# Optimization experiments

Hardware: AMD Instinct MI355X
Metric: run time of the kernel (lower is better)

Reference implementation:

```python
import jax, jax.numpy as jnp
import numpy as np

# static config (matches init_kwargs and a standard 4-level FPN for ~800px input)
SPATIAL_SHAPES = ((100, 100), (50, 50), (25, 25), (13, 13))  # (H_l, W_l)
B, C, H, L, P = 2, 256, 8, 4, 4
DFFN = 2048
DH = C // H
LQ = sum(h * w for h, w in SPATIAL_SHAPES)  # 13294


def layer_norm(x, g, b, eps=1e-5):
    m = jnp.mean(x, -1, keepdims=True)
    v = jnp.mean((x - m) ** 2, -1, keepdims=True)
    return (x - m) * jax.lax.rsqrt(v + eps) * g + b


def ms_deform_sample(value, loc, attn):
    # value [B,Lv,H,DH], loc [B,Lq,H,L,P,2] in [0,1], attn [B,Lq,H,L,P]
    value = jnp.transpose(value, (0, 2, 1, 3))  # [B,H,Lv,DH]
    lq = loc.shape[1]
    out = jnp.zeros((B, H, lq, DH), value.dtype)
    start = 0
    for l, (Hl, Wl) in enumerate(SPATIAL_SHAPES):
        v = jax.lax.dynamic_slice_in_dim(value, start, Hl * Wl, axis=2)  # [B,H,N_l,DH]
        # grid_sample(align_corners=False) coords: x = loc_x*W - 0.5
        gx = jnp.transpose(loc[:, :, :, l, :, 0], (0, 2, 1, 3)) * Wl - 0.5  # [B,H,Lq,P]
        gy = jnp.transpose(loc[:, :, :, l, :, 1], (0, 2, 1, 3)) * Hl - 0.5
        aw = jnp.transpose(attn[:, :, :, l, :], (0, 2, 1, 3))  # [B,H,Lq,P]
        x0 = jnp.floor(gx)
        y0 = jnp.floor(gy)
        for dx in (0.0, 1.0):
            for dy in (0.0, 1.0):
                xi = x0 + dx
                yi = y0 + dy
                w = (1.0 - jnp.abs(gx - xi)) * (1.0 - jnp.abs(gy - yi))
                valid = (xi >= 0) & (xi < Wl) & (yi >= 0) & (yi < Hl)
                idx = (jnp.clip(yi, 0, Hl - 1) * Wl + jnp.clip(xi, 0, Wl - 1)).astype(jnp.int32)
                g = jnp.take_along_axis(v, idx.reshape(B, H, -1)[..., None], axis=2)  # [B,H,Lq*P,DH]
                ww = (w * aw * valid.astype(w.dtype))[..., None]  # [B,H,Lq,P,1]
                out = out + jnp.sum(g.reshape(B, H, lq, P, DH) * ww, axis=3)
        start += Hl * Wl
    return jnp.transpose(out, (0, 2, 1, 3)).reshape(B, lq, C)


def setup_inputs() -> dict:
    key = jax.random.key(0)
    ks = jax.random.split(key, 16)
    s = 0.02
    return {
        "src": jax.random.normal(ks[0], (B, LQ, C), jnp.float32),
        "pos": jax.random.normal(ks[1], (B, LQ, C), jnp.float32),
        "reference_points": jax.random.uniform(ks[2], (B, LQ, L, 2), jnp.float32),
        "w_value": jax.random.normal(ks[3], (C, C), jnp.float32) * s,
        "b_value": jnp.zeros((C,), jnp.float32),
        "w_off": jax.random.normal(ks[4], (C, H * L * P * 2), jnp.float32) * s,
        "b_off": jax.random.normal(ks[5], (H * L * P * 2,), jnp.float32) * s,
        "w_attn": jax.random.normal(ks[6], (C, H * L * P), jnp.float32) * s,
        "b_attn": jnp.zeros((H * L * P,), jnp.float32),
        "w_out": jax.random.normal(ks[7], (C, C), jnp.float32) * s,
        "b_out": jnp.zeros((C,), jnp.float32),
        "ln1_g": jnp.ones((C,), jnp.float32),
        "ln1_b": jnp.zeros((C,), jnp.float32),
        "w_ffn1": jax.random.normal(ks[8], (C, DFFN), jnp.float32) * s,
        "b_ffn1": jnp.zeros((DFFN,), jnp.float32),
        "w_ffn2": jax.random.normal(ks[9], (DFFN, C), jnp.float32) * s,
        "b_ffn2": jnp.zeros((C,), jnp.float32),
        "ln2_g": jnp.ones((C,), jnp.float32),
        "ln2_b": jnp.zeros((C,), jnp.float32),
    }


def reference(src, pos, reference_points, w_value, b_value, w_off, b_off, w_attn, b_attn,
              w_out, b_out, ln1_g, ln1_b, w_ffn1, b_ffn1, w_ffn2, b_ffn2, ln2_g, ln2_b):
    # DeformableTransformerEncoderLayer.forward (eval mode, no dropout)
    q = src + pos  # with_pos_embed
    lq = q.shape[1]
    value = (src @ w_value + b_value).reshape(B, -1, H, DH)
    off = (q @ w_off + b_off).reshape(B, lq, H, L, P, 2)
    attn = (q @ w_attn + b_attn).reshape(B, lq, H, L * P)
    attn = jax.nn.softmax(attn, axis=-1).reshape(B, lq, H, L, P)
    # offset_normalizer = (W_l, H_l)
    norm = jnp.array([[w, h] for h, w in SPATIAL_SHAPES], dtype=src.dtype)
    loc = reference_points[:, :, None, :, None, :] + off / norm[None, None, None, :, None, :]
    src2 = ms_deform_sample(value, loc, attn) @ w_out + b_out
    x = layer_norm(src + src2, ln1_g, ln1_b)
    ff = jax.nn.relu(x @ w_ffn1 + b_ffn1) @ w_ffn2 + b_ffn2
    return layer_norm(x + ff, ln2_g, ln2_b)
```

## Files before the change

kernel.cpp:

```cpp
#include <hip/hip_runtime.h>

#define LQN   13294
#define NBAT  2
#define MROWS (NBAT * LQN)
#define CCH   256
#define NHEAD 8
#define DHEAD 32
#define NLVL  4
#define NPT   4
#define DFF   2048

typedef short short8 __attribute__((ext_vector_type(8)));
typedef float f32x4 __attribute__((ext_vector_type(4)));
typedef unsigned short u16;
typedef u16 u16x4 __attribute__((ext_vector_type(4)));

__device__ __forceinline__ u16 f2bf(float f) {
  unsigned int u = __builtin_bit_cast(unsigned int, f);
  u += 0x7fffu + ((u >> 16) & 1u);
  return (u16)(u >> 16);
}
__device__ __forceinline__ float bf2f(u16 s) {
  unsigned int u = ((unsigned int)s) << 16;
  return __builtin_bit_cast(float, u);
}
__device__ __forceinline__ void async16(const void* g, void* l) {
  __builtin_amdgcn_global_load_lds(
      (const __attribute__((address_space(1))) void*)g,
      (__attribute__((address_space(3))) void*)l, 16, 0, 0);
}

template<int OUT_MODE>
__global__ __launch_bounds__(256, 2)
void gemm_bf16(const u16* __restrict__ A, const u16* __restrict__ BT,
               const float* __restrict__ bias, void* __restrict__ Cout,
               int M, int N, int K)
{
  __shared__ u16 As[2][128 * 64];
  __shared__ u16 Bs[2][128 * 64];
  const int t    = threadIdx.x;
  const int lane = t & 63;
  const int wid  = t >> 6;
  const int wm   = wid >> 1, wn = wid & 1;
  const int bm   = blockIdx.x, bn = blockIdx.y;
  const int l15  = lane & 15;
  const int kq   = lane >> 4;

  f32x4 acc[4][4];
#pragma unroll
  for (int m = 0; m < 4; ++m)
#pragma unroll
    for (int n = 0; n < 4; ++n) acc[m][n] = (f32x4)0.0f;

  auto stage = [&](int buf, int kt) {
#pragma unroll
    for (int i = 0; i < 4; ++i) {
      const int c   = i * 256 + t;
      const int row = c >> 3;
      const int kg  = (c & 7) ^ (row & 7);
      int ar = bm * 128 + row; ar = ar < M ? ar : M - 1;
      async16(&A[(size_t)ar * K + kt + kg * 8], &As[buf][c * 8]);
      const int br = bn * 128 + row;
      async16(&BT[(size_t)br * K + kt + kg * 8], &Bs[buf][c * 8]);
    }
  };

  stage(0, 0);
  __syncthreads();
  int cur = 0;

  for (int kt = 0; kt < K; kt += 64) {
    if (kt + 64 < K) stage(cur ^ 1, kt + 64);

#pragma unroll
    for (int kk = 0; kk < 2; ++kk) {
      short8 af[4], bfr[4];
#pragma unroll
      for (int m = 0; m < 4; ++m) {
        const int row = wm * 64 + m * 16 + l15;
        const int xb  = (kk * 64 + kq * 16) ^ ((row & 7) << 4);
        af[m] = *(const short8*)((const char*)&As[cur][0] + row * 128 + xb);
      }
#pragma unroll
      for (int n = 0; n < 4; ++n) {
        const int col = wn * 64 + n * 16 + l15;
        const int xb  = (kk * 64 + kq * 16) ^ ((col & 7) << 4);
        bfr[n] = *(const short8*)((const char*)&Bs[cur][0] + col * 128 + xb);
      }
#pragma unroll
      for (int m = 0; m < 4; ++m)
#pragma unroll
        for (int n = 0; n < 4; ++n)
          acc[m][n] = __builtin_amdgcn_mfma_f32_16x16x32_bf16(af[m], bfr[n], acc[m][n], 0, 0, 0);
    }

    __syncthreads();
    cur ^= 1;
  }

  const int crow0 = bm * 128 + wm * 64;
  const int ccol0 = bn * 128 + wn * 64;
#pragma unroll
  for (int n = 0; n < 4; ++n) {
    int col = ccol0 + n * 16 + l15;
    float bv = bias[col];
#pragma unroll
    for (int m = 0; m < 4; ++m) {
      int rbase = crow0 + m * 16 + kq * 4;
#pragma unroll
      for (int j = 0; j < 4; ++j) {
        int row = rbase + j;
        if (row < M) {
          float v = acc[m][n][j] + bv;
          if constexpr (OUT_MODE == 0) {
            ((float*)Cout)[(size_t)row * N + col] = v;
          } else {
            if constexpr (OUT_MODE == 2) v = fmaxf(v, 0.0f);
            ((u16*)Cout)[(size_t)row * N + col] = f2bf(v);
          }
        }
      }
    }
  }
}

__global__ __launch_bounds__(512, 2)
void ffn_fused(const u16* __restrict__ x_bf, const u16* __restrict__ W1T,
               const u16* __restrict__ W2T, const float* __restrict__ b1,
               const float* __restrict__ b2, float* __restrict__ out)
{
  extern __shared__ char smem[];
  u16* w1s = (u16*)(smem);
  u16* w2s = (u16*)(smem + 65536);
  char* ps = (char*)(smem + 131072);

  const int t    = threadIdx.x;
  const int lane = t & 63;
  const int wid  = t >> 6;
  const int l15  = lane & 15;
  const int kq   = lane >> 4;
  const int bm   = blockIdx.x;
  const int pwm  = wid >> 1, pwn = wid & 1;
  const int wm   = wid >> 2, wn = wid & 3;

  short8 xr[2][8];
#pragma unroll
  for (int m = 0; m < 2; ++m) {
    int ar = bm * 128 + pwm * 32 + m * 16 + l15;
    ar = ar < MROWS ? ar : MROWS - 1;
    const char* xb = (const char*)x_bf + (size_t)ar * 512 + kq * 16;
#pragma unroll
    for (int ks = 0; ks < 8; ++ks)
      xr[m][ks] = *(const short8*)(xb + ks * 64);
  }

  auto stage = [&](int buf, int it) {
#pragma unroll
    for (int i = 0; i < 4; ++i) {
      const int c  = i * 512 + t;
      const int r1 = c >> 5;
      const int k1 = ((c & 31) ^ (r1 & 7)) * 8;
      async16(&W1T[(size_t)(it * 64 + r1) * 256 + k1], &w1s[buf * 16384 + c * 8]);
      const int r2 = c >> 3;
      const int k2 = ((c & 7) ^ (r2 & 7)) * 8;
      async16(&W2T[(size_t)r2 * 2048 + it * 64 + k2], &w2s[buf * 16384 + c * 8]);
    }
  };

  f32x4 acc[4][4];
#pragma unroll
  for (int m = 0; m < 4; ++m)
#pragma unroll
    for (int n = 0; n < 4; ++n) acc[m][n] = (f32x4)0.0f;

  stage(0, 0);
  __syncthreads();

  for (int it = 0; it < 32; ++it) {
    const int cur = it & 1;
    if (it < 31) stage(cur ^ 1, it + 1);

    f32x4 p[2][2];
#pragma unroll
    for (int m = 0; m < 2; ++m)
#pragma unroll
      for (int n = 0; n < 2; ++n) p[m][n] = (f32x4)0.0f;

#pragma unroll
    for (int ks = 0; ks < 8; ++ks) {
      short8 bfr[2];
#pragma unroll
      for (int n = 0; n < 2; ++n) {
        const int wrow = pwn * 32 + n * 16 + l15;
        const int xb   = (ks * 64 + kq * 16) ^ ((wrow & 7) << 4);
        bfr[n] = *(const short8*)((const char*)&w1s[cur * 16384] + wrow * 512 + xb);
      }
#pragma unroll
      for (int m = 0; m < 2; ++m)
#pragma unroll
        for (int n = 0; n < 2; ++n)
          p[m][n] = __builtin_amdgcn_mfma_f32_16x16x32_bf16(xr[m][ks], bfr[n], p[m][n], 0, 0, 0);
    }

#pragma unroll
    for (int n = 0; n < 2; ++n) {
      const int col = pwn * 32 + n * 16 + l15;
      const float bv = b1[it * 64 + col];
      const int chnk = col >> 3;
      const int sub  = (col & 7) * 2;
#pragma unroll
      for (int m = 0; m < 2; ++m)
#pragma unroll
        for (int j = 0; j < 4; ++j) {
          const int prow = pwm * 32 + m * 16 + kq * 4 + j;
          const float v = fmaxf(p[m][n][j] + bv, 0.0f);
          *(u16*)(ps + prow * 160 + ((chnk ^ ((prow >> 2) & 3)) << 4) + sub) = f2bf(v);
        }
    }
    __syncthreads();

#pragma unroll
    for (int kk = 0; kk < 2; ++kk) {
      short8 paf[4], bfr[4];
#pragma unroll
      for (int m = 0; m < 4; ++m) {
        const int arow = wm * 64 + m * 16 + l15;
        const int c    = kk * 4 + kq;
        paf[m] = *(const short8*)(ps + arow * 160 + ((c ^ ((arow >> 2) & 3)) << 4));
      }
#pragma unroll
      for (int n = 0; n < 4; ++n) {
        const int brow = wn * 64 + n * 16 + l15;
        const int xb   = ((kk * 4 + kq) ^ (brow & 7)) * 16;
        bfr[n] = *(const short8*)((const char*)&w2s[cur * 16384] + brow * 128 + xb);
      }
#pragma unroll
      for (int m = 0; m < 4; ++m)
#pragma unroll
        for (int n = 0; n < 4; ++n)
          acc[m][n] = __builtin_amdgcn_mfma_f32_16x16x32_bf16(paf[m], bfr[n], acc[m][n], 0, 0, 0);
    }
    __syncthreads();
  }

  const int crow0 = bm * 128 + wm * 64;
#pragma unroll
  for (int n = 0; n < 4; ++n) {
    const int col = wn * 64 + n * 16 + l15;
    const float bv = b2[col];
#pragma unroll
    for (int m = 0; m < 4; ++m) {
      const int rbase = crow0 + m * 16 + kq * 4;
#pragma unroll
      for (int j = 0; j < 4; ++j) {
        const int row = rbase + j;
        if (row < MROWS) out[(size_t)row * 256 + col] = acc[m][n][j] + bv;
      }
    }
  }
}

__global__ __launch_bounds__(256)
void sampler_kernel(const float* __restrict__ offattn,
                    const float* __restrict__ refp,
                    const u16*  __restrict__ value,
                    u16*        __restrict__ src2)
{
  __shared__ float2 sWI[2][8][65];

  const int t   = threadIdx.x;
  const int r2  = t >> 7;
  const int g   = t & 127;
  const int row = blockIdx.x * 2 + r2;
  const int b   = row / LQN;

  {
    const int h   = g >> 4;
    const int p16 = g & 15;
    const int l   = p16 >> 2;

    const float* oa = offattn + (size_t)row * 384;

    float logit = oa[256 + h * 16 + p16];
    float mx = logit;
#pragma unroll
    for (int o = 1; o < 16; o <<= 1) mx = fmaxf(mx, __shfl_xor(mx, o, 64));
    float e = __expf(logit - mx);
    float s = e;
#pragma unroll
    for (int o = 1; o < 16; o <<= 1) s += __shfl_xor(s, o, 64);
    const float aw = e / s;

    const int Wl = (l == 0) ? 100 : (l == 1) ? 50 : (l == 2) ? 25 : 13;
    const int Hl = Wl;
    const int st = (l == 0) ? 0 : (l == 1) ? 10000 : (l == 2) ? 12500 : 13125;

    const float ox = oa[(h * 16 + p16) * 2 + 0];
    const float oy = oa[(h * 16 + p16) * 2 + 1];
    const float rx = refp[(size_t)row * 8 + l * 2 + 0] * (float)Wl - 0.5f;
    const float ry = refp[(size_t)row * 8 + l * 2 + 1] * (float)Hl - 0.5f;
    const float gx = rx + ox;
    const float gy = ry + oy;
    const float x0f = floorf(gx), y0f = floorf(gy);
    const int   x0 = (int)x0f, y0 = (int)y0f;
    const float fx = gx - x0f, fy = gy - y0f;

#pragma unroll
    for (int c = 0; c < 4; ++c) {
      const int dx = c & 1, dy = c >> 1;
      const int xi = x0 + dx, yi = y0 + dy;
      const float wx = dx ? fx : 1.0f - fx;
      const float wy = dy ? fy : 1.0f - fy;
      const bool valid = (xi >= 0) && (xi < Wl) && (yi >= 0) && (yi < Hl);
      const int xc = min(max(xi, 0), Wl - 1);
      const int yc = min(max(yi, 0), Hl - 1);
      const int idx = st + yc * Wl + xc;
      const float w = wx * wy * aw * (valid ? 1.0f : 0.0f);
      sWI[r2][h][p16 * 4 + c] = make_float2(w, __builtin_bit_cast(float, idx));
    }
  }
  __syncthreads();

  {
    const int h  = g >> 4;
    const int c2 = g & 15;
    const char* vbase = (const char*)value + (size_t)b * LQN * 512 + h * 64 + c2 * 4;
    const float2* wi = sWI[r2][h];

    float acc0 = 0.f, acc1 = 0.f;
#pragma unroll 16
    for (int e = 0; e < 64; ++e) {
      const float2 p = wi[e];
      const float w  = p.x;
      const int  idx = __builtin_bit_cast(int, p.y);
      const unsigned u = *(const unsigned*)(vbase + (size_t)idx * 512);
      const float f0 = __builtin_bit_cast(float, u << 16);
      const float f1 = __builtin_bit_cast(float, u & 0xffff0000u);
      acc0 += f0 * w;
      acc1 += f1 * w;
    }
    const unsigned o = (unsigned)f2bf(acc0) | ((unsigned)f2bf(acc1) << 16);
    *(unsigned*)&src2[(size_t)row * 256 + h * 32 + c2 * 2] = o;
  }
}

template<int WRITE_BF>
__global__ __launch_bounds__(256)
void ln_kernel(const float* __restrict__ Xa, const float* __restrict__ Xb,
               const float* __restrict__ gam, const float* __restrict__ bet,
               float* __restrict__ Yf, u16* __restrict__ Ybf)
{
  const int wid = threadIdx.x >> 6, lane = threadIdx.x & 63;
  const int row = blockIdx.x * 4 + wid;
  const f32x4 va = ((const f32x4*)(Xa + (size_t)row * 256))[lane];
  const f32x4 vb = ((const f32x4*)(Xb + (size_t)row * 256))[lane];
  f32x4 v = va + vb;
  float s1 = v[0] + v[1] + v[2] + v[3];
  float s2 = v[0] * v[0] + v[1] * v[1] + v[2] * v[2] + v[3] * v[3];
#pragma unroll
  for (int off = 32; off; off >>= 1) {
    s1 += __shfl_xor(s1, off, 64);
    s2 += __shfl_xor(s2, off, 64);
  }
  const float mean = s1 * (1.0f / 256.0f);
  const float var  = s2 * (1.0f / 256.0f) - mean * mean;
  const float rstd = rsqrtf(var + 1e-5f);
  const f32x4 gv = ((const f32x4*)gam)[lane];
  const f32x4 bv = ((const f32x4*)bet)[lane];
  f32x4 y;
#pragma unroll
  for (int j = 0; j < 4; ++j) y[j] = (v[j] - mean) * rstd * gv[j] + bv[j];
  ((f32x4*)(Yf + (size_t)row * 256))[lane] = y;
  if constexpr (WRITE_BF) {
    u16x4 o;
#pragma unroll
    for (int j = 0; j < 4; ++j) o[j] = f2bf(y[j]);
    ((u16x4*)(Ybf + (size_t)row * 256))[lane] = o;
  }
}

__global__ __launch_bounds__(256)
void prep_qsrc(const float* __restrict__ src, const float* __restrict__ pos,
               u16* __restrict__ src_bf, u16* __restrict__ q_bf)
{
  const size_t i = (size_t)blockIdx.x * 256 + threadIdx.x;
  const f32x4 s = ((const f32x4*)src)[i];
  const f32x4 p = ((const f32x4*)pos)[i];
  u16x4 sb, qb;
#pragma unroll
  for (int j = 0; j < 4; ++j) { sb[j] = f2bf(s[j]); qb[j] = f2bf(s[j] + p[j]); }
  ((u16x4*)src_bf)[i] = sb;
  ((u16x4*)q_bf)[i]   = qb;
}

__global__ __launch_bounds__(256)
void transpose_cast(const float* __restrict__ W, u16* __restrict__ WT, int K, int N)
{
  const int i = blockIdx.x * 256 + threadIdx.x;
  if (i >= K * N) return;
  const int k = i / N, n = i - k * N;
  WT[(size_t)n * K + k] = f2bf(W[i]);
}

__global__ __launch_bounds__(256)
void concat_bias(const float* __restrict__ b_off, const float* __restrict__ b_attn,
                 float* __restrict__ out)
{
  const int i = blockIdx.x * 256 + threadIdx.x;
  if (i < 256) out[i] = b_off[i];
  else if (i < 384) out[i] = b_attn[i - 256];
}

extern "C" void kernel_launch(void* const* d_in, const int* in_sizes, int n_in,
                              void* d_out, int out_size, void* d_ws, size_t ws_size,
                              hipStream_t stream)
{
  const float* src     = (const float*)d_in[0];
  const float* pos     = (const float*)d_in[1];
  const float* refp    = (const float*)d_in[2];
  const float* w_value = (const float*)d_in[3];
  const float* b_value = (const float*)d_in[4];
  const float* w_off   = (const float*)d_in[5];
  const float* b_off   = (const float*)d_in[6];
  const float* w_attn  = (const float*)d_in[7];
  const float* b_attn  = (const float*)d_in[8];
  const float* w_out   = (const float*)d_in[9];
  const float* b_out   = (const float*)d_in[10];
  const float* ln1_g   = (const float*)d_in[11];
  const float* ln1_b   = (const float*)d_in[12];
  const float* w_ffn1  = (const float*)d_in[13];
  const float* b_ffn1  = (const float*)d_in[14];
  const float* w_ffn2  = (const float*)d_in[15];
  const float* b_ffn2  = (const float*)d_in[16];
  const float* ln2_g   = (const float*)d_in[17];
  const float* ln2_b   = (const float*)d_in[18];

  char* ws = (char*)d_ws;
  size_t off = 0;
  auto alloc = [&](size_t bytes) { void* p = ws + off; off += (bytes + 255) & ~(size_t)255; return p; };

  u16*   src_bf   = (u16*)  alloc((size_t)MROWS * 256 * 2);
  u16*   q_bf     = (u16*)  alloc((size_t)MROWS * 256 * 2);
  float* offattn  = (float*)alloc((size_t)MROWS * 384 * 4);
  u16*   value_bf = (u16*)  alloc((size_t)MROWS * 256 * 2);
  u16*   src2_bf  = (u16*)  alloc((size_t)MROWS * 256 * 2);
  float* x_f32    = (float*)alloc((size_t)MROWS * 256 * 4);
  u16*   WT_val   = (u16*)  alloc(256 * 256 * 2);
  u16*   WT_oa    = (u16*)  alloc(384 * 256 * 2);
  u16*   WT_out   = (u16*)  alloc(256 * 256 * 2);
  u16*   WT_f1    = (u16*)  alloc(2048 * 256 * 2);
  u16*   WT_f2    = (u16*)  alloc((size_t)256 * 2048 * 2);
  float* bias_oa  = (float*)alloc(384 * 4);

  float* src2p = offattn;
  u16*   x_bf  = q_bf;
  float* ff    = (float*)value_bf;

  transpose_cast<<<256, 256, 0, stream>>>(w_value, WT_val, 256, 256);
  transpose_cast<<<256, 256, 0, stream>>>(w_off, WT_oa, 256, 256);
  transpose_cast<<<128, 256, 0, stream>>>(w_attn, WT_oa + 256 * 256, 256, 128);
  transpose_cast<<<256, 256, 0, stream>>>(w_out, WT_out, 256, 256);
  transpose_cast<<<2048, 256, 0, stream>>>(w_ffn1, WT_f1, 256, 2048);
  transpose_cast<<<2048, 256, 0, stream>>>(w_ffn2, WT_f2, 2048, 256);
  concat_bias<<<2, 256, 0, stream>>>(b_off, b_attn, bias_oa);

  prep_qsrc<<<6647, 256, 0, stream>>>(src, pos, src_bf, q_bf);

  gemm_bf16<1><<<dim3(208, 2), 256, 0, stream>>>(src_bf, WT_val, b_value, value_bf, MROWS, 256, 256);
  gemm_bf16<0><<<dim3(208, 3), 256, 0, stream>>>(q_bf, WT_oa, bias_oa, offattn, MROWS, 384, 256);

  sampler_kernel<<<MROWS / 2, 256, 0, stream>>>(offattn, refp, value_bf, src2_bf);

  gemm_bf16<0><<<dim3(208, 2), 256, 0, stream>>>(src2_bf, WT_out, b_out, src2p, MROWS, 256, 256);

  ln_kernel<1><<<6647, 256, 0, stream>>>(src, src2p, ln1_g, ln1_b, x_f32, x_bf);

  static bool attr_set = false;
  if (!attr_set) {
    hipFuncSetAttribute((const void*)ffn_fused,
                        hipFuncAttributeMaxDynamicSharedMemorySize, 151552);
    attr_set = true;
  }
  ffn_fused<<<208, 512, 151552, stream>>>(x_bf, WT_f1, WT_f2, b_ffn1, b_ffn2, ff);

  ln_kernel<0><<<6647, 256, 0, stream>>>(x_f32, ff, ln2_g, ln2_b, (float*)d_out, nullptr);
}
```

Baseline: 252.3 us.

## Software-pipeline FFN with W2 in registers; load full K=256 tiles in GEMM

The fused FFN kernel is restructured into a skewed two-stage pipeline. The P=relu(xW1) tile for step i is computed while the PV accumulation for step i-1 runs, using double-buffered P tiles in shared memory, and W2 fragments are loaded straight from global memory into registers instead of being staged in LDS. This removes one barrier per iteration and cuts LDS use, at the cost of more registers and unswizzled padded P stores. The small K=256 GEMMs now load the whole K extent into 128KB of shared memory in one shot with no k-loop double buffering, which drops occupancy to one block per CU.

```diff
diff --git a/kernel.cpp b/kernel.cpp
--- a/kernel.cpp
+++ b/kernel.cpp
@@ -31,13 +31,15 @@
 }
 
 template<int OUT_MODE>
-__global__ __launch_bounds__(256, 2)
-void gemm_bf16(const u16* __restrict__ A, const u16* __restrict__ BT,
+__global__ __launch_bounds__(256, 1)
+void gemm_k256(const u16* __restrict__ A, const u16* __restrict__ BT,
                const float* __restrict__ bias, void* __restrict__ Cout,
-               int M, int N, int K)
-{
-  __shared__ u16 As[2][128 * 64];
-  __shared__ u16 Bs[2][128 * 64];
+               int M, int N)
+{
+  extern __shared__ char smem[];
+  char* As = smem;
+  char* Bs = smem + 65536;
+
   const int t    = threadIdx.x;
   const int lane = t & 63;
   const int wid  = t >> 6;
@@ -46,56 +48,43 @@
   const int l15  = lane & 15;
   const int kq   = lane >> 4;
 
+#pragma unroll
+  for (int i = 0; i < 16; ++i) {
+    const int c   = i * 256 + t;
+    const int row = c >> 5;
+    const int kgE = ((c & 31) ^ (row & 7)) * 8;
+    int ar = bm * 128 + row; ar = ar < M ? ar : M - 1;
+    async16(&A[(size_t)ar * 256 + kgE], As + c * 16);
+    const int br = bn * 128 + row;
+    async16(&BT[(size_t)br * 256 + kgE], Bs + c * 16);
+  }
+
   f32x4 acc[4][4];
 #pragma unroll
   for (int m = 0; m < 4; ++m)
 #pragma unroll
     for (int n = 0; n < 4; ++n) acc[m][n] = (f32x4)0.0f;
 
-  auto stage = [&](int buf, int kt) {
-#pragma unroll
-    for (int i = 0; i < 4; ++i) {
-      const int c   = i * 256 + t;
-      const int row = c >> 3;
-      const int kg  = (c & 7) ^ (row & 7);
-      int ar = bm * 128 + row; ar = ar < M ? ar : M - 1;
-      async16(&A[(size_t)ar * K + kt + kg * 8], &As[buf][c * 8]);
-      const int br = bn * 128 + row;
-      async16(&BT[(size_t)br * K + kt + kg * 8], &Bs[buf][c * 8]);
-    }
-  };
-
-  stage(0, 0);
   __syncthreads();
-  int cur = 0;
-
-  for (int kt = 0; kt < K; kt += 64) {
-    if (kt + 64 < K) stage(cur ^ 1, kt + 64);
-
-#pragma unroll
-    for (int kk = 0; kk < 2; ++kk) {
-      short8 af[4], bfr[4];
-#pragma unroll
-      for (int m = 0; m < 4; ++m) {
-        const int row = wm * 64 + m * 16 + l15;
-        const int xb  = (kk * 64 + kq * 16) ^ ((row & 7) << 4);
-        af[m] = *(const short8*)((const char*)&As[cur][0] + row * 128 + xb);
-      }
-#pragma unroll
-      for (int n = 0; n < 4; ++n) {
-        const int col = wn * 64 + n * 16 + l15;
-        const int xb  = (kk * 64 + kq * 16) ^ ((col & 7) << 4);
-        bfr[n] = *(const short8*)((const char*)&Bs[cur][0] + col * 128 + xb);
-      }
-#pragma unroll
-      for (int m = 0; m < 4; ++m)
-#pragma unroll
-        for (int n = 0; n < 4; ++n)
-          acc[m][n] = __builtin_amdgcn_mfma_f32_16x16x32_bf16(af[m], bfr[n], acc[m][n], 0, 0, 0);
-    }
-
-    __syncthreads();
-    cur ^= 1;
+
+#pragma unroll
+  for (int ks = 0; ks < 8; ++ks) {
+    short8 af[4], bfr[4];
+#pragma unroll
+    for (int m = 0; m < 4; ++m) {
+      const int row = wm * 64 + m * 16 + l15;
+      af[m] = *(const short8*)(As + row * 512 + (((ks * 4 + kq) ^ (row & 7)) << 4));
+    }
+#pragma unroll
+    for (int n = 0; n < 4; ++n) {
+      const int col = wn * 64 + n * 16 + l15;
+      bfr[n] = *(const short8*)(Bs + col * 512 + (((ks * 4 + kq) ^ (col & 7)) << 4));
+    }
+#pragma unroll
+    for (int m = 0; m < 4; ++m)
+#pragma unroll
+      for (int n = 0; n < 4; ++n)
+        acc[m][n] = __builtin_amdgcn_mfma_f32_16x16x32_bf16(af[m], bfr[n], acc[m][n], 0, 0, 0);
   }
 
   const int crow0 = bm * 128 + wm * 64;
@@ -112,12 +101,8 @@
         int row = rbase + j;
         if (row < M) {
           float v = acc[m][n][j] + bv;
-          if constexpr (OUT_MODE == 0) {
-            ((float*)Cout)[(size_t)row * N + col] = v;
-          } else {
-            if constexpr (OUT_MODE == 2) v = fmaxf(v, 0.0f);
-            ((u16*)Cout)[(size_t)row * N + col] = f2bf(v);
-          }
+          if constexpr (OUT_MODE == 0) ((float*)Cout)[(size_t)row * N + col] = v;
+          else                         ((u16*)Cout)[(size_t)row * N + col] = f2bf(v);
         }
       }
     }
@@ -130,9 +115,10 @@
                const float* __restrict__ b2, float* __restrict__ out)
 {
   extern __shared__ char smem[];
-  u16* w1s = (u16*)(smem);
-  u16* w2s = (u16*)(smem + 65536);
-  char* ps = (char*)(smem + 131072);
+  u16*  w1s0 = (u16*)(smem);
+  u16*  w1s1 = (u16*)(smem + 32768);
+  char* ps0  = smem + 65536;
+  char* ps1  = smem + 65536 + 21504;
 
   const int t    = threadIdx.x;
   const int lane = t & 63;
@@ -154,16 +140,13 @@
       xr[m][ks] = *(const short8*)(xb + ks * 64);
   }
 
-  auto stage = [&](int buf, int it) {
+  auto stage_w1 = [&](u16* buf, int it) {
 #pragma unroll
     for (int i = 0; i < 4; ++i) {
       const int c  = i * 512 + t;
       const int r1 = c >> 5;
       const int k1 = ((c & 31) ^ (r1 & 7)) * 8;
-      async16(&W1T[(size_t)(it * 64 + r1) * 256 + k1], &w1s[buf * 16384 + c * 8]);
-      const int r2 = c >> 3;
-      const int k2 = ((c & 7) ^ (r2 & 7)) * 8;
-      async16(&W2T[(size_t)r2 * 2048 + it * 64 + k2], &w2s[buf * 16384 + c * 8]);
+      async16(&W1T[(size_t)(it * 64 + r1) * 256 + k1], &buf[c * 8]);
     }
   };
 
@@ -173,75 +156,85 @@
 #pragma unroll
     for (int n = 0; n < 4; ++n) acc[m][n] = (f32x4)0.0f;
 
-  stage(0, 0);
+  short8 w2rA[2][4], w2rB[2][4];
+
+  auto body = [&](int i, bool doPV, bool doP,
+                  short8 (&w2u)[2][4], short8 (&w2l)[2][4],
+                  const u16* w1u, u16* w1stg, char* psR, char* psW) {
+    if (doP) {
+#pragma unroll
+      for (int kk = 0; kk < 2; ++kk)
+#pragma unroll
+        for (int n = 0; n < 4; ++n) {
+          const int brow = wn * 64 + n * 16 + l15;
+          w2l[kk][n] = *(const short8*)&W2T[(size_t)brow * 2048 + i * 64 + kk * 32 + kq * 8];
+        }
+      if (i < 31) stage_w1(w1stg, i + 1);
+
+      f32x4 p[2][2];
+#pragma unroll
+      for (int m = 0; m < 2; ++m)
+#pragma unroll
+        for (int n = 0; n < 2; ++n) p[m][n] = (f32x4)0.0f;
+#pragma unroll
+      for (int ks = 0; ks < 8; ++ks) {
+        short8 bfr[2];
+#pragma unroll
+        for (int n = 0; n < 2; ++n) {
+          const int wrow = pwn * 32 + n * 16 + l15;
+          const int xb   = (ks * 64 + kq * 16) ^ ((wrow & 7) << 4);
+          bfr[n] = *(const short8*)((const char*)w1u + wrow * 512 + xb);
+        }
+#pragma unroll
+        for (int m = 0; m < 2; ++m)
+#pragma unroll
+          for (int n = 0; n < 2; ++n)
+            p[m][n] = __builtin_amdgcn_mfma_f32_16x16x32_bf16(xr[m][ks], bfr[n], p[m][n], 0, 0, 0);
+      }
+#pragma unroll
+      for (int n = 0; n < 2; ++n) {
+        const int col = pwn * 32 + n * 16 + l15;
+        const float bv = b1[i * 64 + col];
+#pragma unroll
+        for (int m = 0; m < 2; ++m)
+#pragma unroll
+          for (int j = 0; j < 4; ++j) {
+            const int prow = pwm * 32 + m * 16 + kq * 4 + j;
+            *(u16*)(psW + prow * 168 + col * 2) = f2bf(fmaxf(p[m][n][j] + bv, 0.0f));
+          }
+      }
+    }
+
+    if (doPV) {
+#pragma unroll
+      for (int kk = 0; kk < 2; ++kk) {
+        short8 paf[4];
+#pragma unroll
+        for (int m = 0; m < 4; ++m) {
+          const int arow = wm * 64 + m * 16 + l15;
+          paf[m] = *(const short8*)(psR + arow * 168 + (kk * 4 + kq) * 16);
+        }
+#pragma unroll
+        for (int m = 0; m < 4; ++m)
+#pragma unroll
+          for (int n = 0; n < 4; ++n)
+            acc[m][n] = __builtin_amdgcn_mfma_f32_16x16x32_bf16(paf[m], w2u[kk][n], acc[m][n], 0, 0, 0);
+      }
+    }
+
+    if (doP) __syncthreads();
+  };
+
+  stage_w1(w1s0, 0);
   __syncthreads();
 
-  for (int it = 0; it < 32; ++it) {
-    const int cur = it & 1;
-    if (it < 31) stage(cur ^ 1, it + 1);
-
-    f32x4 p[2][2];
-#pragma unroll
-    for (int m = 0; m < 2; ++m)
-#pragma unroll
-      for (int n = 0; n < 2; ++n) p[m][n] = (f32x4)0.0f;
-
-#pragma unroll
-    for (int ks = 0; ks < 8; ++ks) {
-      short8 bfr[2];
-#pragma unroll
-      for (int n = 0; n < 2; ++n) {
-        const int wrow = pwn * 32 + n * 16 + l15;
-        const int xb   = (ks * 64 + kq * 16) ^ ((wrow & 7) << 4);
-        bfr[n] = *(const short8*)((const char*)&w1s[cur * 16384] + wrow * 512 + xb);
-      }
-#pragma unroll
-      for (int m = 0; m < 2; ++m)
-#pragma unroll
-        for (int n = 0; n < 2; ++n)
-          p[m][n] = __builtin_amdgcn_mfma_f32_16x16x32_bf16(xr[m][ks], bfr[n], p[m][n], 0, 0, 0);
-    }
-
-#pragma unroll
-    for (int n = 0; n < 2; ++n) {
-      const int col = pwn * 32 + n * 16 + l15;
-      const float bv = b1[it * 64 + col];
-      const int chnk = col >> 3;
-      const int sub  = (col & 7) * 2;
-#pragma unroll
-      for (int m = 0; m < 2; ++m)
-#pragma unroll
-        for (int j = 0; j < 4; ++j) {
-          const int prow = pwm * 32 + m * 16 + kq * 4 + j;
-          const float v = fmaxf(p[m][n][j] + bv, 0.0f);
-          *(u16*)(ps + prow * 160 + ((chnk ^ ((prow >> 2) & 3)) << 4) + sub) = f2bf(v);
-        }
-    }
-    __syncthreads();
-
-#pragma unroll
-    for (int kk = 0; kk < 2; ++kk) {
-      short8 paf[4], bfr[4];
-#pragma unroll
-      for (int m = 0; m < 4; ++m) {
-        const int arow = wm * 64 + m * 16 + l15;
-        const int c    = kk * 4 + kq;
-        paf[m] = *(const short8*)(ps + arow * 160 + ((c ^ ((arow >> 2) & 3)) << 4));
-      }
-#pragma unroll
-      for (int n = 0; n < 4; ++n) {
-        const int brow = wn * 64 + n * 16 + l15;
-        const int xb   = ((kk * 4 + kq) ^ (brow & 7)) * 16;
-        bfr[n] = *(const short8*)((const char*)&w2s[cur * 16384] + brow * 128 + xb);
-      }
-#pragma unroll
-      for (int m = 0; m < 4; ++m)
-#pragma unroll
-        for (int n = 0; n < 4; ++n)
-          acc[m][n] = __builtin_amdgcn_mfma_f32_16x16x32_bf16(paf[m], bfr[n], acc[m][n], 0, 0, 0);
-    }
-    __syncthreads();
-  }
+  body(0, false, true, w2rB, w2rA, w1s0, w1s1, ps1, ps0);
+  for (int tt = 0; tt < 15; ++tt) {
+    body(2 * tt + 1, true, true, w2rA, w2rB, w1s1, w1s0, ps0, ps1);
+    body(2 * tt + 2, true, true, w2rB, w2rA, w1s0, w1s1, ps1, ps0);
+  }
+  body(31, true, true, w2rA, w2rB, w1s1, w1s0, ps0, ps1);
+  body(32, true, false, w2rB, w2rA, w1s0, w1s1, ps1, ps0);
 
   const int crow0 = bm * 128 + wm * 64;
 #pragma unroll
@@ -466,22 +459,27 @@
 
   prep_qsrc<<<6647, 256, 0, stream>>>(src, pos, src_bf, q_bf);
 
-  gemm_bf16<1><<<dim3(208, 2), 256, 0, stream>>>(src_bf, WT_val, b_value, value_bf, MROWS, 256, 256);
-  gemm_bf16<0><<<dim3(208, 3), 256, 0, stream>>>(q_bf, WT_oa, bias_oa, offattn, MROWS, 384, 256);
-
-  sampler_kernel<<<MROWS / 2, 256, 0, stream>>>(offattn, refp, value_bf, src2_bf);
-
-  gemm_bf16<0><<<dim3(208, 2), 256, 0, stream>>>(src2_bf, WT_out, b_out, src2p, MROWS, 256, 256);
-
-  ln_kernel<1><<<6647, 256, 0, stream>>>(src, src2p, ln1_g, ln1_b, x_f32, x_bf);
-
   static bool attr_set = false;
   if (!attr_set) {
     hipFuncSetAttribute((const void*)ffn_fused,
-                        hipFuncAttributeMaxDynamicSharedMemorySize, 151552);
+                        hipFuncAttributeMaxDynamicSharedMemorySize, 110592);
+    hipFuncSetAttribute((const void*)gemm_k256<0>,
+                        hipFuncAttributeMaxDynamicSharedMemorySize, 131072);
+    hipFuncSetAttribute((const void*)gemm_k256<1>,
+                        hipFuncAttributeMaxDynamicSharedMemorySize, 131072);
     attr_set = true;
   }
-  ffn_fused<<<208, 512, 151552, stream>>>(x_bf, WT_f1, WT_f2, b_ffn1, b_ffn2, ff);
+
+  gemm_k256<1><<<dim3(208, 2), 256, 131072, stream>>>(src_bf, WT_val, b_value, value_bf, MROWS, 256);
+  gemm_k256<0><<<dim3(208, 3), 256, 131072, stream>>>(q_bf, WT_oa, bias_oa, offattn, MROWS, 384);
+
+  sampler_kernel<<<MROWS / 2, 256, 0, stream>>>(offattn, refp, value_bf, src2_bf);
+
+  gemm_k256<0><<<dim3(208, 2), 256, 131072, stream>>>(src2_bf, WT_out, b_out, src2p, MROWS, 256);
+
+  ln_kernel<1><<<6647, 256, 0, stream>>>(src, src2p, ln1_g, ln1_b, x_f32, x_bf);
+
+  ffn_fused<<<208, 512, 108544, stream>>>(x_bf, WT_f1, WT_f2, b_ffn1, b_ffn2, ff);
 
   ln_kernel<0><<<6647, 256, 0, stream>>>(x_f32, ff, ln2_g, ln2_b, (float*)d_out, nullptr);
 }
```

Result: slower. 386.6 us (+53.2%).
